# Kernel optimization log

Measured on AMD Instinct MI355X. Metric: run time of the kernel, lower is better.

## Reference

```python
import jax, jax.numpy as jnp
import numpy as np

N_NODES = 10000
DEG = 32            # max_edges (fixed degree after padding)
CHANNELS = 16
IN_DIM = 4
BATCH = 8


def setup_inputs() -> dict:
    key = jax.random.key(0)
    k1, k2, k3 = jax.random.split(key, 3)
    E = N_NODES * DEG
    x = jax.random.normal(k1, (BATCH, N_NODES, IN_DIM), dtype=jnp.float32)
    # neighbor indices in [0, N_NODES]; index N_NODES is the padded 'useless' zero node
    edges = jax.random.randint(k2, (E,), 0, N_NODES + 1, dtype=jnp.int64)
    # torch.rand init: uniform [0,1); one weight tensor per input channel
    weights = jax.random.uniform(k3, (IN_DIM, E, CHANNELS), dtype=jnp.float32)
    return {"x": x, "edges": edges, "weights": weights}


def reference(x, edges, weights):
    B, N, in_dim = x.shape
    E = edges.shape[0]
    deg = E // N
    C = weights.shape[-1]
    # append zero 'useless node' so padding index N gathers zeros
    x_pad = jnp.concatenate([x, jnp.zeros((B, 1, in_dim), dtype=x.dtype)], axis=1)  # [B, N+1, in_dim]
    # super_edges = cat([edges]*C); viewed as [E, C] row-major (matches torch .view)
    idx = jnp.tile(edges, C).reshape(E, C)  # [E, C]
    out = jnp.zeros((B, N, C), dtype=x.dtype)
    for i in range(in_dim):  # small fixed loop over input channels (distinct weights)
        g = x_pad[:, :, i]              # [B, N+1]
        toc = g[:, idx]                 # gather -> [B, E, C]
        conv = toc * weights[i]         # per-edge weights broadcast over batch
        out = out + conv.reshape(B, N, deg, C).sum(axis=2)  # fixed-window segment sum
    return out
```

## Files before the change

kernel.cpp:

```cpp
#include <hip/hip_runtime.h>
#include <hip/hip_bf16.h>

#define N_NODES 10000
#define DEG     32
#define CH      16
#define IN_DIM  4
#define BATCH   8
#define E_EDGES (N_NODES * DEG)
#define WI_STRIDE (E_EDGES * CH)
#define P_COUNT 625

__global__ __launch_bounds__(256) void lcg_transpose(const float* __restrict__ x,
                                                     float* __restrict__ xt) {
    int t = blockIdx.x * 256 + threadIdx.x;
    if (t < BATCH * N_NODES) {
        int b = t / N_NODES;
        int node = t - b * N_NODES;
        float4 v = *(const float4*)(x + 4 * t);
        *(float4*)(xt + node * 32 + b * 4) = v;
    } else if (t < BATCH * N_NODES + 8) {
        int r = t - BATCH * N_NODES;
        *(float4*)(xt + N_NODES * 32 + r * 4) = make_float4(0.f, 0.f, 0.f, 0.f);
    }
}

__global__ __launch_bounds__(256, 4) void lcg_main(
    const float* __restrict__ xt,
    const int*   __restrict__ edges,
    const float* __restrict__ w,
    float*       __restrict__ out)
{
    __shared__ float lx[256 * 36];

    int bid = blockIdx.x;
    int p  = bid >> 1;
    int ch = bid & 1;
    int t  = threadIdx.x;

    {
        int sub  = t & 7;
        int sidx = t >> 3;
        int nd[8];
#pragma unroll
        for (int k = 0; k < 8; k++) {
            int s = sidx + 32 * k;
            int d = s >> 3, c_l = s & 7;
            nd[k] = edges[512 * p + 16 * d + 8 * ch + c_l];
        }
#pragma unroll
        for (int k = 0; k < 8; k++) {
            int s = sidx + 32 * k;
            float4 v = *(const float4*)(xt + nd[k] * 32 + sub * 4);
            *(float4*)(&lx[s * 36 + sub * 4]) = v;
        }
    }
    __syncthreads();

    int c_l = t & 7;
    int bh  = (t >> 3) & 1;
    int j   = t >> 4;
    int n   = p + P_COUNT * j;
    int c   = ch * 8 + c_l;

    const float* wp = w + (n * DEG) * CH + c;
    float acc0 = 0.f, acc1 = 0.f, acc2 = 0.f, acc3 = 0.f;

#pragma unroll 4
    for (int d = 0; d < DEG; d++) {
        float w0 = wp[d * CH];
        float w1 = wp[d * CH + WI_STRIDE];
        float w2 = wp[d * CH + 2 * WI_STRIDE];
        float w3 = wp[d * CH + 3 * WI_STRIDE];
        const float* lp = &lx[(d * 8 + c_l) * 36 + 16 * bh];
        float4 x0 = *(const float4*)(lp);
        float4 x1 = *(const float4*)(lp + 4);
        float4 x2 = *(const float4*)(lp + 8);
        float4 x3 = *(const float4*)(lp + 12);
        acc0 += x0.x * w0 + x0.y * w1 + x0.z * w2 + x0.w * w3;
        acc1 += x1.x * w0 + x1.y * w1 + x1.z * w2 + x1.w * w3;
        acc2 += x2.x * w0 + x2.y * w1 + x2.z * w2 + x2.w * w3;
        acc3 += x3.x * w0 + x3.y * w1 + x3.z * w2 + x3.w * w3;
    }

    int ob = n * CH + c;
    out[(4 * bh + 0) * (N_NODES * CH) + ob] = acc0;
    out[(4 * bh + 1) * (N_NODES * CH) + ob] = acc1;
    out[(4 * bh + 2) * (N_NODES * CH) + ob] = acc2;
    out[(4 * bh + 3) * (N_NODES * CH) + ob] = acc3;
}

extern "C" void kernel_launch(void* const* d_in, const int* in_sizes, int n_in,
                              void* d_out, int out_size, void* d_ws, size_t ws_size,
                              hipStream_t stream) {
    const float* x     = (const float*)d_in[0];
    const int*   edges = (const int*)d_in[1];
    const float* w     = (const float*)d_in[2];
    float* out = (float*)d_out;
    float* xt  = (float*)d_ws;

    int tr_total  = BATCH * N_NODES + 8;
    int tr_blocks = (tr_total + 255) / 256;
    lcg_transpose<<<tr_blocks, 256, 0, stream>>>(x, xt);

    lcg_main<<<2 * P_COUNT, 256, 0, stream>>>(xt, edges, w, out);
}
```

Measured before the change: 133.4 us.

## Handle all 16 channels and 8 batches per thread block, halving block count

Each block now covers all 16 channels of its 16 nodes instead of splitting channels across two blocks. Each thread accumulates all 8 batch outputs, so each weight is loaded once per thread rather than twice across batch halves. Weight loads and output stores use nontemporal hints to avoid cache pollution. The trade-off is double the shared memory, more registers, lower occupancy (launch bound 2) and only 625 blocks, which reduces parallelism.

```diff
diff --git a/kernel.cpp b/kernel.cpp
--- a/kernel.cpp
+++ b/kernel.cpp
@@ -9,6 +9,7 @@
 #define E_EDGES (N_NODES * DEG)
 #define WI_STRIDE (E_EDGES * CH)
 #define P_COUNT 625
+#define LX_STRIDE 36
 
 __global__ __launch_bounds__(256) void lcg_transpose(const float* __restrict__ x,
                                                      float* __restrict__ xt) {
@@ -24,69 +25,61 @@
     }
 }
 
-__global__ __launch_bounds__(256, 4) void lcg_main(
+__global__ __launch_bounds__(256, 2) void lcg_main(
     const float* __restrict__ xt,
     const int*   __restrict__ edges,
     const float* __restrict__ w,
     float*       __restrict__ out)
 {
-    __shared__ float lx[256 * 36];
+    __shared__ float lx[512 * LX_STRIDE];
 
-    int bid = blockIdx.x;
-    int p  = bid >> 1;
-    int ch = bid & 1;
-    int t  = threadIdx.x;
+    int p = blockIdx.x;
+    int t = threadIdx.x;
 
     {
-        int sub  = t & 7;
-        int sidx = t >> 3;
-        int nd[8];
+        int sub = t & 7;
+        int rg  = t >> 3;
+        const int* ep = edges + 512 * p;
+        int nd[16];
 #pragma unroll
-        for (int k = 0; k < 8; k++) {
-            int s = sidx + 32 * k;
-            int d = s >> 3, c_l = s & 7;
-            nd[k] = edges[512 * p + 16 * d + 8 * ch + c_l];
-        }
+        for (int k = 0; k < 16; k++) nd[k] = ep[rg + 32 * k];
 #pragma unroll
-        for (int k = 0; k < 8; k++) {
-            int s = sidx + 32 * k;
+        for (int k = 0; k < 16; k++) {
+            int s = rg + 32 * k;
             float4 v = *(const float4*)(xt + nd[k] * 32 + sub * 4);
-            *(float4*)(&lx[s * 36 + sub * 4]) = v;
+            *(float4*)(&lx[s * LX_STRIDE + sub * 4]) = v;
         }
     }
     __syncthreads();
 
-    int c_l = t & 7;
-    int bh  = (t >> 3) & 1;
-    int j   = t >> 4;
-    int n   = p + P_COUNT * j;
-    int c   = ch * 8 + c_l;
+    int c = t & 15;
+    int j = t >> 4;
+    int n = p + P_COUNT * j;
 
     const float* wp = w + (n * DEG) * CH + c;
-    float acc0 = 0.f, acc1 = 0.f, acc2 = 0.f, acc3 = 0.f;
+    float acc[BATCH];
+#pragma unroll
+    for (int b = 0; b < BATCH; b++) acc[b] = 0.0f;
 
-#pragma unroll 4
+#pragma unroll 2
     for (int d = 0; d < DEG; d++) {
-        float w0 = wp[d * CH];
-        float w1 = wp[d * CH + WI_STRIDE];
-        float w2 = wp[d * CH + 2 * WI_STRIDE];
-        float w3 = wp[d * CH + 3 * WI_STRIDE];
-        const float* lp = &lx[(d * 8 + c_l) * 36 + 16 * bh];
-        float4 x0 = *(const float4*)(lp);
-        float4 x1 = *(const float4*)(lp + 4);
-        float4 x2 = *(const float4*)(lp + 8);
-        float4 x3 = *(const float4*)(lp + 12);
-        acc0 += x0.x * w0 + x0.y * w1 + x0.z * w2 + x0.w * w3;
-        acc1 += x1.x * w0 + x1.y * w1 + x1.z * w2 + x1.w * w3;
-        acc2 += x2.x * w0 + x2.y * w1 + x2.z * w2 + x2.w * w3;
-        acc3 += x3.x * w0 + x3.y * w1 + x3.z * w2 + x3.w * w3;
+        float w0 = __builtin_nontemporal_load(wp + d * CH);
+        float w1 = __builtin_nontemporal_load(wp + d * CH + WI_STRIDE);
+        float w2 = __builtin_nontemporal_load(wp + d * CH + 2 * WI_STRIDE);
+        float w3 = __builtin_nontemporal_load(wp + d * CH + 3 * WI_STRIDE);
+        const float* lp = &lx[(16 * d + c) * LX_STRIDE];
+        float4 xv[BATCH];
+#pragma unroll
+        for (int b = 0; b < BATCH; b++) xv[b] = *(const float4*)(lp + 4 * b);
+#pragma unroll
+        for (int b = 0; b < BATCH; b++)
+            acc[b] += xv[b].x * w0 + xv[b].y * w1 + xv[b].z * w2 + xv[b].w * w3;
     }
 
     int ob = n * CH + c;
-    out[(4 * bh + 0) * (N_NODES * CH) + ob] = acc0;
-    out[(4 * bh + 1) * (N_NODES * CH) + ob] = acc1;
-    out[(4 * bh + 2) * (N_NODES * CH) + ob] = acc2;
-    out[(4 * bh + 3) * (N_NODES * CH) + ob] = acc3;
+#pragma unroll
+    for (int b = 0; b < BATCH; b++)
+        __builtin_nontemporal_store(acc[b], out + b * (N_NODES * CH) + ob);
 }
 
 extern "C" void kernel_launch(void* const* d_in, const int* in_sizes, int n_in,
@@ -102,5 +95,5 @@
     int tr_blocks = (tr_total + 255) / 256;
     lcg_transpose<<<tr_blocks, 256, 0, stream>>>(x, xt);
 
-    lcg_main<<<2 * P_COUNT, 256, 0, stream>>>(xt, edges, w, out);
+    lcg_main<<<P_COUNT, 256, 0, stream>>>(xt, edges, w, out);
 }
```

Result: slower. 141.0 us (+5.8%).
